# Performance work log

Hardware: AMD Instinct MI355X
Metric: run time of the kernel (lower is better)

Reference implementation:

```python
import jax, jax.numpy as jnp
import numpy as np

K = 9          # number of umbrella neighbors (excluding self)
BN_EPS = 1e-5


def setup_inputs() -> dict:
    key = jax.random.key(0)
    ks = jax.random.split(key, 8)
    B, N, C = 4, 8192, 3
    ch = 7
    x = jax.random.normal(ks[0], (B, N, C), jnp.float32)
    w1 = jax.random.normal(ks[1], (ch, ch), jnp.float32) * 0.4
    gamma1 = jnp.ones((ch,), jnp.float32)
    beta1 = jnp.zeros((ch,), jnp.float32)
    w2 = jax.random.normal(ks[2], (ch, ch), jnp.float32) * 0.4
    bias2 = jax.random.normal(ks[3], (ch,), jnp.float32) * 0.1
    gamma2 = jnp.ones((ch,), jnp.float32)
    beta2 = jnp.zeros((ch,), jnp.float32)
    w3 = jax.random.normal(ks[4], (ch, ch), jnp.float32) * 0.4
    bias3 = jax.random.normal(ks[5], (ch,), jnp.float32) * 0.1
    return dict(x=x, w1=w1, gamma1=gamma1, beta1=beta1, w2=w2, bias2=bias2,
                gamma2=gamma2, beta2=beta2, w3=w3, bias3=bias3)


def _bn(t, gamma, beta):
    # BatchNorm2d in training mode: batch stats over (B, N, K) per channel (last dim)
    m = t.mean(axis=(0, 1, 2))
    v = t.var(axis=(0, 1, 2))  # biased, matching torch BN normalization
    return (t - m) * jax.lax.rsqrt(v + BN_EPS) * gamma + beta


def reference(x, w1, gamma1, beta1, w2, bias2, gamma2, beta2, w3, bias3):
    B, N, _ = x.shape
    # ---- kNN (negative squared distance, top-k largest == nearest) ----
    xsq = jnp.sum(x * x, axis=-1)                       # [B,N]
    xx = jnp.einsum('bnc,bmc->bnm', x, x)               # [B,N,N]
    dist = 2.0 * xx - xsq[:, :, None] - xsq[:, None, :]
    idx = jax.lax.top_k(dist, K + 1)[1]                 # [B,N,K+1], includes self
    # ---- gather neighbor coords, recenter, drop self ----
    nbr = jax.vmap(lambda xb, ib: xb[ib])(x, idx)       # [B,N,K+1,3]
    nbr = nbr - x[:, :, None, :]
    nbr = nbr[:, :, 1:, :]                              # [B,N,K,3]
    # ---- sort neighbors by azimuth phi ----
    phi = jnp.arctan2(nbr[..., 1], nbr[..., 0]) / (2.0 * np.pi) + 0.5
    order = jnp.argsort(phi, axis=-1)                   # [B,N,K]
    srt = jnp.take_along_axis(nbr, order[..., None], axis=2)  # [B,N,K,3]
    # ---- umbrella pairs: (v_i, v_{i+1 mod K}) ----
    v1 = srt
    v2 = jnp.roll(srt, -1, axis=2)
    centroids = 0.5 * (v1 + v2)                         # [B,N,K,3]
    normals = jnp.cross(v1, v2) + 1e-5
    normals = normals / jnp.linalg.norm(normals, axis=-1, keepdims=True)
    # flip so the first normal's x-component is positive (per point)
    pos_mask = (normals[:, :, 0:1, 0] > 0).astype(x.dtype) * 2.0 - 1.0  # [B,N,1]
    normals = normals * pos_mask[..., None]
    positions = jnp.sum(centroids * normals, axis=-1) / jnp.sqrt(jnp.asarray(3.0, x.dtype))
    feat = jnp.concatenate([centroids, normals, positions[..., None]], axis=-1)  # [B,N,K,7]
    # ---- tiny 1x1 conv MLP (channel-last einsum) + BN + ReLU ----
    h = jnp.einsum('bnkc,oc->bnko', feat, w1)
    h = jax.nn.relu(_bn(h, gamma1, beta1))
    h = jnp.einsum('bnkc,oc->bnko', h, w2) + bias2
    h = jax.nn.relu(_bn(h, gamma2, beta2))
    h = jnp.einsum('bnkc,oc->bnko', h, w3) + bias3
    pooled = jnp.max(h, axis=2)                         # [B,N,7]
    return jnp.concatenate([x, pooled], axis=-1)        # [B,N,10]
```

## Files before the change

kernel.cpp:

```cpp
#include <hip/hip_runtime.h>
#include <math.h>

#define BB 4
#define NN 8192
#define TOTAL (BB*NN)
#define KNBR 9
#define CH 7
#define NCHUNK 16
#define CHUNK (NN/NCHUNK)
#define SLOTS 8
#define NROWS (NCHUNK*SLOTS/2)
#define QB 4
#define BN_EPS 1e-5f
#define M_ELEMS (TOTAL*KNBR)
#define NREP 16
#define NBLK 256

#define OFF_PTS   0
#define OFF_PI    524288
#define OFF_STATS 8912896

__device__ __forceinline__ void ibody(float (&dl)[10], int (&il)[10], float d, int ii) {
    bool c0 = d > dl[0];
#pragma unroll
    for (int p = 9; p > 0; p--) {
        bool here = d > dl[p];
        bool up   = d > dl[p-1];
        float nd = up ? dl[p-1] : d;
        int   ni = up ? il[p-1] : ii;
        if (here) { dl[p] = nd; il[p] = ni; }
    }
    if (c0) { dl[0] = d; il[0] = ii; }
}

__device__ __forceinline__ void insert10(float (&dl)[10], int (&il)[10], float d, int ii) {
    if (d > dl[9]) ibody(dl, il, d, ii);
}

__global__ __launch_bounds__(256) void knn_k(const float* __restrict__ x,
                                             float4* __restrict__ pts,
                                             unsigned int* __restrict__ pi,
                                             float* __restrict__ stats) {
    const int b = blockIdx.z, chunk = blockIdx.y;
    const int c0 = chunk * CHUNK;

    if (blockIdx.x == 0 && blockIdx.y == 0 && blockIdx.z == 0) {
        for (int i = threadIdx.x; i < NREP*28 + 8; i += 256) stats[i] = 0.f;
    }

    __shared__ float4 tile[CHUNK];
    if (threadIdx.x < CHUNK/4) {
        const float4* __restrict__ x4 = (const float4*)(x + (long)(b*NN + c0)*3);
        int t = threadIdx.x;
        float4 f0 = x4[3*t], f1 = x4[3*t+1], f2 = x4[3*t+2];
        float px[4] = {f0.x, f0.w, f1.z, f2.y};
        float py[4] = {f0.y, f1.x, f1.w, f2.z};
        float pz[4] = {f0.z, f1.y, f2.x, f2.w};
#pragma unroll
        for (int u = 0; u < 4; u++) {
            float sq = __fadd_rn(__fadd_rn(__fmul_rn(px[u],px[u]), __fmul_rn(py[u],py[u])),
                                 __fmul_rn(pz[u],pz[u]));
            tile[4*t+u] = make_float4(px[u], py[u], pz[u], sq);
        }
    }
    __syncthreads();

    if (blockIdx.x == 0) {
#pragma unroll
        for (int j = 0; j < CHUNK/256; j++)
            pts[b*NN + c0 + threadIdx.x + j*256] = tile[threadIdx.x + j*256];
    }

    const int q0 = blockIdx.x * (256*QB) + threadIdx.x;
    float qx2[QB], qy2[QB], qz2[QB], nqb[QB];
#pragma unroll
    for (int v = 0; v < QB; v++) {
        long qoff = (long)(b*NN + q0 + v*256) * 3;
        float qx = x[qoff], qy = x[qoff+1], qz = x[qoff+2];
        float qw = qx*qx + qy*qy + qz*qz;
        qx2[v] = qx + qx; qy2[v] = qy + qy; qz2[v] = qz + qz;
        nqb[v] = -1.0f - qw;
    }

    unsigned int m[QB][SLOTS];
#pragma unroll
    for (int v = 0; v < QB; v++)
#pragma unroll
        for (int s = 0; s < SLOTS; s++) m[v][s] = 0xFFFFFFFFu;

#pragma unroll 4
    for (int j = 0; j < CHUNK; j++) {
        float4 t = tile[j];
#pragma unroll
        for (int v = 0; v < QB; v++) {
            float d = fmaf(qx2[v], t.x, fmaf(qy2[v], t.y, fmaf(qz2[v], t.z, nqb[v] - t.w)));
            unsigned int kd = (__float_as_uint(d) & 0xFFFFFE00u) | (unsigned int)j;
#pragma unroll
            for (int p = SLOTS-1; p >= 1; p--)
                asm("v_med3_u32 %0, %1, %2, %3" : "=v"(m[v][p]) : "v"(kd), "v"(m[v][p-1]), "v"(m[v][p]));
            m[v][0] = kd < m[v][0] ? kd : m[v][0];
        }
    }

#pragma unroll
    for (int v = 0; v < QB; v++) {
        int idx[SLOTS];
#pragma unroll
        for (int s = 0; s < SLOTS; s++) idx[s] = (int)(m[v][s] & 511u);
#pragma unroll
        for (int r = 0; r < SLOTS; r++) {
#pragma unroll
            for (int i = (r & 1); i + 1 < SLOTS; i += 2) {
                int a = idx[i], c = idx[i+1];
                idx[i] = min(a, c); idx[i+1] = max(a, c);
            }
        }
        int g = b*NN + q0 + v*256;
#pragma unroll
        for (int s2 = 0; s2 < SLOTS/2; s2++) {
            unsigned int lo = (unsigned int)(c0 + idx[2*s2]);
            unsigned int hi = (unsigned int)(c0 + idx[2*s2+1]);
            pi[(long)(chunk*(SLOTS/2) + s2)*TOTAL + g] = lo | (hi << 16);
        }
    }
}

__device__ __forceinline__ void grid_barrier(int* cnt) {
    __syncthreads();
    if (threadIdx.x == 0) {
        __threadfence();
        __hip_atomic_fetch_add(cnt, 1, __ATOMIC_RELEASE, __HIP_MEMORY_SCOPE_AGENT);
        while (__hip_atomic_load(cnt, __ATOMIC_ACQUIRE, __HIP_MEMORY_SCOPE_AGENT) < NBLK)
            __builtin_amdgcn_s_sleep(8);
    }
    __syncthreads();
}

__global__ __launch_bounds__(128, 1) void fused_k(const float* __restrict__ x,
                                                  const float4* __restrict__ pts,
                                                  const unsigned int* __restrict__ pi,
                                                  const float* __restrict__ w1,
                                                  const float* __restrict__ gamma1, const float* __restrict__ beta1,
                                                  const float* __restrict__ w2, const float* __restrict__ bias2,
                                                  const float* __restrict__ gamma2, const float* __restrict__ beta2,
                                                  const float* __restrict__ w3, const float* __restrict__ bias3,
                                                  float* __restrict__ stats, float* __restrict__ out) {
    __shared__ float sw1[49], sw2[49], sw3[49], sb2[7], sb3[7];
    __shared__ float acc[14];
    __shared__ float sco[14];
    if (threadIdx.x < 49) {
        sw1[threadIdx.x] = w1[threadIdx.x];
        sw2[threadIdx.x] = w2[threadIdx.x];
        sw3[threadIdx.x] = w3[threadIdx.x];
    }
    if (threadIdx.x < 7) { sb2[threadIdx.x] = bias2[threadIdx.x]; sb3[threadIdx.x] = bias3[threadIdx.x]; }
    if (threadIdx.x < 14) acc[threadIdx.x] = 0.f;
    __syncthreads();

    int* cnt = (int*)(stats + NREP*28);
    int g = blockIdx.x * 128 + threadIdx.x;
    int b = g >> 13, n = g & (NN-1);
    const float4* __restrict__ base = pts + b*NN;
    float4 qp = base[n];
    float qn = -qp.w;

    float dl[10]; int il[10];
#pragma unroll
    for (int j = 0; j < 10; j++) { dl[j] = -INFINITY; il[j] = 0; }
#pragma unroll
    for (int h = 0; h < 2; h++) {
        unsigned int pk[32];
#pragma unroll
        for (int u = 0; u < 32; u++) pk[u] = pi[(long)(h*32 + u)*TOTAL + g];
#pragma unroll
        for (int bt = 0; bt < 4; bt++) {
            int id[16];
#pragma unroll
            for (int u = 0; u < 8; u++) {
                id[2*u]   = (int)(pk[bt*8 + u] & 0xFFFFu);
                id[2*u+1] = (int)(pk[bt*8 + u] >> 16);
            }
            float4 pp[16];
#pragma unroll
            for (int v = 0; v < 16; v++) pp[v] = base[id[v]];
            float dd[16];
#pragma unroll
            for (int v = 0; v < 16; v++) {
                float dot2 = __fadd_rn(__fadd_rn(__fmul_rn(qp.x, 2.f*pp[v].x),
                                                 __fmul_rn(qp.y, 2.f*pp[v].y)),
                                       __fmul_rn(qp.z, 2.f*pp[v].z));
                dd[v] = __fsub_rn(__fadd_rn(dot2, qn), pp[v].w);
            }
#pragma unroll
            for (int v = 0; v < 16; v++) insert10(dl, il, dd[v], id[v]);
        }
    }

    float vx[9], vy[9], vz[9], ph[9];
#pragma unroll
    for (int t = 0; t < 9; t++) {
        float4 p4 = base[il[t+1]];
        vx[t] = p4.x - qp.x; vy[t] = p4.y - qp.y; vz[t] = p4.z - qp.z;
        ph[t] = atan2f(vy[t], vx[t]) / 6.283185307179586f + 0.5f;
    }

    int rank[9];
#pragma unroll
    for (int t = 0; t < 9; t++) {
        int r = 0;
#pragma unroll
        for (int u = 0; u < 9; u++) {
            if (u == t) continue;
            bool before = (ph[u] < ph[t]) || (ph[u] == ph[t] && u < t);
            r += before ? 1 : 0;
        }
        rank[t] = r;
    }
    float sx[9], sy[9], sz[9];
#pragma unroll
    for (int s = 0; s < 9; s++) {
        float a = 0.f, bb = 0.f, c = 0.f;
#pragma unroll
        for (int t = 0; t < 9; t++) {
            bool m = (rank[t] == s);
            a = m ? vx[t] : a; bb = m ? vy[t] : bb; c = m ? vz[t] : c;
        }
        sx[s] = a; sy[s] = bb; sz[s] = c;
    }

    float sgn;
    {
        float ax = sx[0], ay = sy[0], az = sz[0];
        float bx = sx[1], by = sy[1], bz = sz[1];
        float nx0 = ay*bz - az*by + 1e-5f;
        float ny0 = az*bx - ax*bz + 1e-5f;
        float nz0 = ax*by - ay*bx + 1e-5f;
        float inv = 1.0f / sqrtf(nx0*nx0 + ny0*ny0 + nz0*nz0);
        sgn = (nx0*inv > 0.0f) ? 1.0f : -1.0f;
    }

    float hv[63];
    float sum[7], sumsq[7];
#pragma unroll
    for (int o = 0; o < 7; o++) { sum[o] = 0.f; sumsq[o] = 0.f; }

#pragma unroll
    for (int t = 0; t < 9; t++) {
        const int t2 = (t + 1) % 9;
        float ax = sx[t],  ay = sy[t],  az = sz[t];
        float bx = sx[t2], by = sy[t2], bz = sz[t2];
        float cx = 0.5f*(ax+bx), cy = 0.5f*(ay+by), cz = 0.5f*(az+bz);
        float nx0 = ay*bz - az*by + 1e-5f;
        float ny0 = az*bx - ax*bz + 1e-5f;
        float nz0 = ax*by - ay*bx + 1e-5f;
        float inv = 1.0f / sqrtf(nx0*nx0 + ny0*ny0 + nz0*nz0);
        float nx = nx0*inv*sgn, ny = ny0*inv*sgn, nz = nz0*inv*sgn;
        float pos = (cx*nx + cy*ny + cz*nz) / 1.7320508075688772f;

        float f[7] = {cx, cy, cz, nx, ny, nz, pos};
#pragma unroll
        for (int o = 0; o < 7; o++) {
            float h = 0.f;
#pragma unroll
            for (int c = 0; c < 7; c++) h += f[c] * sw1[o*7 + c];
            hv[t*7 + o] = h;
            sum[o] += h; sumsq[o] += h*h;
        }
    }

#pragma unroll
    for (int o = 0; o < 7; o++) {
        float s  = sum[o];
        float s2 = sumsq[o];
        for (int off = 32; off > 0; off >>= 1) { s += __shfl_down(s, off); s2 += __shfl_down(s2, off); }
        if ((threadIdx.x & 63) == 0) {
            atomicAdd(&acc[o], s);
            atomicAdd(&acc[7 + o], s2);
        }
    }
    __syncthreads();
    if (threadIdx.x < 14)
        atomicAdd(&stats[(blockIdx.x & (NREP-1))*28 + threadIdx.x], acc[threadIdx.x]);

    grid_barrier(&cnt[0]);

    const float invM = 1.0f / (float)M_ELEMS;
    if (threadIdx.x < 7) {
        int c = threadIdx.x;
        float sm = 0.f, sq = 0.f;
#pragma unroll
        for (int r = 0; r < NREP; r++) {
            sm += __hip_atomic_load(&stats[r*28 + c],     __ATOMIC_RELAXED, __HIP_MEMORY_SCOPE_AGENT);
            sq += __hip_atomic_load(&stats[r*28 + 7 + c], __ATOMIC_RELAXED, __HIP_MEMORY_SCOPE_AGENT);
        }
        float m = sm * invM;
        float v = sq * invM - m*m;
        float sc = gamma1[c] / sqrtf(v + BN_EPS);
        sco[c] = sc; sco[7 + c] = beta1[c] - m*sc;
    }
    if (threadIdx.x >= 64 && threadIdx.x < 78) acc[threadIdx.x - 64] = 0.f;
    __syncthreads();

#pragma unroll
    for (int o = 0; o < 7; o++) { sum[o] = 0.f; sumsq[o] = 0.f; }
#pragma unroll
    for (int t = 0; t < 9; t++) {
        float a[7];
#pragma unroll
        for (int c = 0; c < 7; c++) a[c] = fmaxf(hv[t*7 + c]*sco[c] + sco[7 + c], 0.0f);
#pragma unroll
        for (int o = 0; o < 7; o++) {
            float h = 0.f;
#pragma unroll
            for (int c = 0; c < 7; c++) h += a[c] * sw2[o*7 + c];
            h += sb2[o];
            hv[t*7 + o] = h;
            sum[o] += h; sumsq[o] += h*h;
        }
    }
#pragma unroll
    for (int o = 0; o < 7; o++) {
        float s  = sum[o];
        float s2 = sumsq[o];
        for (int off = 32; off > 0; off >>= 1) { s += __shfl_down(s, off); s2 += __shfl_down(s2, off); }
        if ((threadIdx.x & 63) == 0) {
            atomicAdd(&acc[o], s);
            atomicAdd(&acc[7 + o], s2);
        }
    }
    __syncthreads();
    if (threadIdx.x < 14)
        atomicAdd(&stats[(blockIdx.x & (NREP-1))*28 + 14 + threadIdx.x], acc[threadIdx.x]);

    grid_barrier(&cnt[1]);

    if (threadIdx.x < 7) {
        int c = threadIdx.x;
        float sm = 0.f, sq = 0.f;
#pragma unroll
        for (int r = 0; r < NREP; r++) {
            sm += __hip_atomic_load(&stats[r*28 + 14 + c], __ATOMIC_RELAXED, __HIP_MEMORY_SCOPE_AGENT);
            sq += __hip_atomic_load(&stats[r*28 + 21 + c], __ATOMIC_RELAXED, __HIP_MEMORY_SCOPE_AGENT);
        }
        float m = sm * invM;
        float v = sq * invM - m*m;
        float sc = gamma2[c] / sqrtf(v + BN_EPS);
        sco[c] = sc; sco[7 + c] = beta2[c] - m*sc;
    }
    __syncthreads();

    float pooled[7];
#pragma unroll
    for (int o = 0; o < 7; o++) pooled[o] = -INFINITY;
#pragma unroll
    for (int t = 0; t < 9; t++) {
        float a[7];
#pragma unroll
        for (int c = 0; c < 7; c++) a[c] = fmaxf(hv[t*7 + c]*sco[c] + sco[7 + c], 0.0f);
#pragma unroll
        for (int o = 0; o < 7; o++) {
            float h = 0.f;
#pragma unroll
            for (int c = 0; c < 7; c++) h += a[c] * sw3[o*7 + c];
            h += sb3[o];
            pooled[o] = fmaxf(pooled[o], h);
        }
    }
    out[g*10 + 0] = qp.x;
    out[g*10 + 1] = qp.y;
    out[g*10 + 2] = qp.z;
#pragma unroll
    for (int o = 0; o < 7; o++) out[g*10 + 3 + o] = pooled[o];
}

extern "C" void kernel_launch(void* const* d_in, const int* in_sizes, int n_in,
                              void* d_out, int out_size, void* d_ws, size_t ws_size,
                              hipStream_t stream) {
    const float* x      = (const float*)d_in[0];
    const float* w1     = (const float*)d_in[1];
    const float* gamma1 = (const float*)d_in[2];
    const float* beta1  = (const float*)d_in[3];
    const float* w2     = (const float*)d_in[4];
    const float* bias2  = (const float*)d_in[5];
    const float* gamma2 = (const float*)d_in[6];
    const float* beta2  = (const float*)d_in[7];
    const float* w3     = (const float*)d_in[8];
    const float* bias3  = (const float*)d_in[9];
    float* out = (float*)d_out;

    char* ws = (char*)d_ws;
    float4*       pts  = (float4*)(ws + OFF_PTS);
    unsigned int* pi   = (unsigned int*)(ws + OFF_PI);
    float*        stats= (float*)(ws + OFF_STATS);

    knn_k  <<<dim3(NN/(256*QB), NCHUNK, BB), 256, 0, stream>>>(x, pts, pi, stats);
    fused_k<<<NBLK, 128, 0, stream>>>(x, pts, pi, w1, gamma1, beta1, w2, bias2,
                                      gamma2, beta2, w3, bias3, stats, out);
}
```

Baseline: 244.6 us.

## Split fused kernel at first BN barrier, spilling layer-1 activations to workspace

Splits the persistent fused kernel into a geometry kernel that writes first-layer activations to a global buffer and a tail kernel that does the remaining two layers. The first software grid barrier is replaced by a kernel boundary, and the geometry kernel loses its launch-bound occupancy cap of one block. In exchange it writes and re-reads about 9 MB of activations, and it adds a launch. The tail kernel recomputes the BN1 coefficients per thread from stats instead of sharing them through shared memory.

New measurement: 231.8 us. -5.2%, faster.

```diff
diff --git a/kernel.cpp b/kernel.cpp
--- a/kernel.cpp
+++ b/kernel.cpp
@@ -19,6 +19,7 @@
 #define OFF_PTS   0
 #define OFF_PI    524288
 #define OFF_STATS 8912896
+#define OFF_H1    8914944
 
 __device__ __forceinline__ void ibody(float (&dl)[10], int (&il)[10], float d, int ii) {
     bool c0 = d > dl[0];
@@ -125,39 +126,16 @@
     }
 }
 
-__device__ __forceinline__ void grid_barrier(int* cnt) {
-    __syncthreads();
-    if (threadIdx.x == 0) {
-        __threadfence();
-        __hip_atomic_fetch_add(cnt, 1, __ATOMIC_RELEASE, __HIP_MEMORY_SCOPE_AGENT);
-        while (__hip_atomic_load(cnt, __ATOMIC_ACQUIRE, __HIP_MEMORY_SCOPE_AGENT) < NBLK)
-            __builtin_amdgcn_s_sleep(8);
-    }
-    __syncthreads();
-}
-
-__global__ __launch_bounds__(128, 1) void fused_k(const float* __restrict__ x,
-                                                  const float4* __restrict__ pts,
-                                                  const unsigned int* __restrict__ pi,
-                                                  const float* __restrict__ w1,
-                                                  const float* __restrict__ gamma1, const float* __restrict__ beta1,
-                                                  const float* __restrict__ w2, const float* __restrict__ bias2,
-                                                  const float* __restrict__ gamma2, const float* __restrict__ beta2,
-                                                  const float* __restrict__ w3, const float* __restrict__ bias3,
-                                                  float* __restrict__ stats, float* __restrict__ out) {
-    __shared__ float sw1[49], sw2[49], sw3[49], sb2[7], sb3[7];
+__global__ __launch_bounds__(128) void geom_k(const float4* __restrict__ pts,
+                                              const unsigned int* __restrict__ pi,
+                                              const float* __restrict__ w1,
+                                              float* __restrict__ h1, float* __restrict__ stats) {
+    __shared__ float sw1[49];
     __shared__ float acc[14];
-    __shared__ float sco[14];
-    if (threadIdx.x < 49) {
-        sw1[threadIdx.x] = w1[threadIdx.x];
-        sw2[threadIdx.x] = w2[threadIdx.x];
-        sw3[threadIdx.x] = w3[threadIdx.x];
-    }
-    if (threadIdx.x < 7) { sb2[threadIdx.x] = bias2[threadIdx.x]; sb3[threadIdx.x] = bias3[threadIdx.x]; }
+    if (threadIdx.x < 49) sw1[threadIdx.x] = w1[threadIdx.x];
     if (threadIdx.x < 14) acc[threadIdx.x] = 0.f;
     __syncthreads();
 
-    int* cnt = (int*)(stats + NREP*28);
     int g = blockIdx.x * 128 + threadIdx.x;
     int b = g >> 13, n = g & (NN-1);
     const float4* __restrict__ base = pts + b*NN;
@@ -239,7 +217,6 @@
         sgn = (nx0*inv > 0.0f) ? 1.0f : -1.0f;
     }
 
-    float hv[63];
     float sum[7], sumsq[7];
 #pragma unroll
     for (int o = 0; o < 7; o++) { sum[o] = 0.f; sumsq[o] = 0.f; }
@@ -258,12 +235,13 @@
         float pos = (cx*nx + cy*ny + cz*nz) / 1.7320508075688772f;
 
         float f[7] = {cx, cy, cz, nx, ny, nz, pos};
+        float* outp = h1 + ((long)g*9 + t) * 7;
 #pragma unroll
         for (int o = 0; o < 7; o++) {
             float h = 0.f;
 #pragma unroll
             for (int c = 0; c < 7; c++) h += f[c] * sw1[o*7 + c];
-            hv[t*7 + o] = h;
+            outp[o] = h;
             sum[o] += h; sumsq[o] += h*h;
         }
     }
@@ -281,33 +259,60 @@
     __syncthreads();
     if (threadIdx.x < 14)
         atomicAdd(&stats[(blockIdx.x & (NREP-1))*28 + threadIdx.x], acc[threadIdx.x]);
-
-    grid_barrier(&cnt[0]);
-
+}
+
+__device__ __forceinline__ void grid_barrier(int* cnt) {
+    __syncthreads();
+    if (threadIdx.x == 0) {
+        __threadfence();
+        __hip_atomic_fetch_add(cnt, 1, __ATOMIC_RELEASE, __HIP_MEMORY_SCOPE_AGENT);
+        while (__hip_atomic_load(cnt, __ATOMIC_ACQUIRE, __HIP_MEMORY_SCOPE_AGENT) < NBLK)
+            __builtin_amdgcn_s_sleep(8);
+    }
+    __syncthreads();
+}
+
+__global__ __launch_bounds__(128) void tail_k(const float* __restrict__ x,
+                                              const float* __restrict__ h1,
+                                              const float* __restrict__ gamma1, const float* __restrict__ beta1,
+                                              const float* __restrict__ w2, const float* __restrict__ bias2,
+                                              const float* __restrict__ gamma2, const float* __restrict__ beta2,
+                                              const float* __restrict__ w3, const float* __restrict__ bias3,
+                                              float* __restrict__ stats, float* __restrict__ out) {
+    __shared__ float sw2[49], sw3[49], sb2[7], sb3[7];
+    __shared__ float acc[14];
+    __shared__ float sco[14];
+    if (threadIdx.x < 49) { sw2[threadIdx.x] = w2[threadIdx.x]; sw3[threadIdx.x] = w3[threadIdx.x]; }
+    if (threadIdx.x < 7)  { sb2[threadIdx.x] = bias2[threadIdx.x]; sb3[threadIdx.x] = bias3[threadIdx.x]; }
+    if (threadIdx.x < 14) acc[threadIdx.x] = 0.f;
+    __syncthreads();
+
+    int* cnt = (int*)(stats + NREP*28);
+    int g = blockIdx.x * 128 + threadIdx.x;
     const float invM = 1.0f / (float)M_ELEMS;
-    if (threadIdx.x < 7) {
-        int c = threadIdx.x;
+
+    float s1v[7], b1v[7];
+#pragma unroll
+    for (int c = 0; c < 7; c++) {
         float sm = 0.f, sq = 0.f;
 #pragma unroll
-        for (int r = 0; r < NREP; r++) {
-            sm += __hip_atomic_load(&stats[r*28 + c],     __ATOMIC_RELAXED, __HIP_MEMORY_SCOPE_AGENT);
-            sq += __hip_atomic_load(&stats[r*28 + 7 + c], __ATOMIC_RELAXED, __HIP_MEMORY_SCOPE_AGENT);
-        }
+        for (int r = 0; r < NREP; r++) { sm += stats[r*28 + c]; sq += stats[r*28 + 7 + c]; }
         float m = sm * invM;
         float v = sq * invM - m*m;
         float sc = gamma1[c] / sqrtf(v + BN_EPS);
-        sco[c] = sc; sco[7 + c] = beta1[c] - m*sc;
-    }
-    if (threadIdx.x >= 64 && threadIdx.x < 78) acc[threadIdx.x - 64] = 0.f;
-    __syncthreads();
-
+        s1v[c] = sc; b1v[c] = beta1[c] - m*sc;
+    }
+
+    float hv[63];
+    float sum[7], sumsq[7];
 #pragma unroll
     for (int o = 0; o < 7; o++) { sum[o] = 0.f; sumsq[o] = 0.f; }
+    const float* hh = h1 + (long)g * 63;
 #pragma unroll
     for (int t = 0; t < 9; t++) {
         float a[7];
 #pragma unroll
-        for (int c = 0; c < 7; c++) a[c] = fmaxf(hv[t*7 + c]*sco[c] + sco[7 + c], 0.0f);
+        for (int c = 0; c < 7; c++) a[c] = fmaxf(hh[t*7 + c]*s1v[c] + b1v[c], 0.0f);
 #pragma unroll
         for (int o = 0; o < 7; o++) {
             float h = 0.f;
@@ -332,7 +337,7 @@
     if (threadIdx.x < 14)
         atomicAdd(&stats[(blockIdx.x & (NREP-1))*28 + 14 + threadIdx.x], acc[threadIdx.x]);
 
-    grid_barrier(&cnt[1]);
+    grid_barrier(cnt);
 
     if (threadIdx.x < 7) {
         int c = threadIdx.x;
@@ -366,9 +371,9 @@
             pooled[o] = fmaxf(pooled[o], h);
         }
     }
-    out[g*10 + 0] = qp.x;
-    out[g*10 + 1] = qp.y;
-    out[g*10 + 2] = qp.z;
+    out[g*10 + 0] = x[g*3 + 0];
+    out[g*10 + 1] = x[g*3 + 1];
+    out[g*10 + 2] = x[g*3 + 2];
 #pragma unroll
     for (int o = 0; o < 7; o++) out[g*10 + 3 + o] = pooled[o];
 }
@@ -392,8 +397,10 @@
     float4*       pts  = (float4*)(ws + OFF_PTS);
     unsigned int* pi   = (unsigned int*)(ws + OFF_PI);
     float*        stats= (float*)(ws + OFF_STATS);
-
-    knn_k  <<<dim3(NN/(256*QB), NCHUNK, BB), 256, 0, stream>>>(x, pts, pi, stats);
-    fused_k<<<NBLK, 128, 0, stream>>>(x, pts, pi, w1, gamma1, beta1, w2, bias2,
-                                      gamma2, beta2, w3, bias3, stats, out);
-}
+    float*        h1   = (float*)(ws + OFF_H1);
+
+    knn_k <<<dim3(NN/(256*QB), NCHUNK, BB), 256, 0, stream>>>(x, pts, pi, stats);
+    geom_k<<<TOTAL/128, 128, 0, stream>>>(pts, pi, w1, h1, stats);
+    tail_k<<<NBLK, 128, 0, stream>>>(x, h1, gamma1, beta1, w2, bias2,
+                                     gamma2, beta2, w3, bias3, stats, out);
+}
```

## Merge chunk candidates by packed approximate-distance keys before exact rescoring

Applied to the files above, without the earlier changes.

The kNN kernel now writes each chunk's 8 candidates as full 32-bit keys that hold the truncated distance bits plus a 13-bit global index, instead of sorted packed 16-bit index pairs. The second kernel runs a v_med3 selection network over all 128 keys to keep the best 20, then gathers and exactly rescores only those 20 points instead of all 128. This removes most of the random float4 gathers and exact distance computations. In exchange it doubles the candidate buffer written and read, and it relies on the truncated-key preselection never dropping a true top-10 neighbour.

Result: faster. 233.0 us (-4.7%).

```diff
diff --git a/kernel.cpp b/kernel.cpp
--- a/kernel.cpp
+++ b/kernel.cpp
@@ -9,7 +9,8 @@
 #define NCHUNK 16
 #define CHUNK (NN/NCHUNK)
 #define SLOTS 8
-#define NROWS (NCHUNK*SLOTS/2)
+#define NROWS (NCHUNK*SLOTS)
+#define GSEL 20
 #define QB 4
 #define BN_EPS 1e-5f
 #define M_ELEMS (TOTAL*KNBR)
@@ -18,7 +19,7 @@
 
 #define OFF_PTS   0
 #define OFF_PI    524288
-#define OFF_STATS 8912896
+#define OFF_STATS 17301504
 
 __device__ __forceinline__ void ibody(float (&dl)[10], int (&il)[10], float d, int ii) {
     bool c0 = d > dl[0];
@@ -104,23 +105,12 @@
 
 #pragma unroll
     for (int v = 0; v < QB; v++) {
-        int idx[SLOTS];
-#pragma unroll
-        for (int s = 0; s < SLOTS; s++) idx[s] = (int)(m[v][s] & 511u);
-#pragma unroll
-        for (int r = 0; r < SLOTS; r++) {
-#pragma unroll
-            for (int i = (r & 1); i + 1 < SLOTS; i += 2) {
-                int a = idx[i], c = idx[i+1];
-                idx[i] = min(a, c); idx[i+1] = max(a, c);
-            }
-        }
         int g = b*NN + q0 + v*256;
 #pragma unroll
-        for (int s2 = 0; s2 < SLOTS/2; s2++) {
-            unsigned int lo = (unsigned int)(c0 + idx[2*s2]);
-            unsigned int hi = (unsigned int)(c0 + idx[2*s2+1]);
-            pi[(long)(chunk*(SLOTS/2) + s2)*TOTAL + g] = lo | (hi << 16);
+        for (int s = 0; s < SLOTS; s++) {
+            unsigned int mm = m[v][s];
+            unsigned int key = (mm & 0xFFFFE000u) | (unsigned int)(c0 + (int)(mm & 511u));
+            pi[(long)(chunk*SLOTS + s)*TOTAL + g] = key;
         }
     }
 }
@@ -136,15 +126,15 @@
     __syncthreads();
 }
 
-__global__ __launch_bounds__(128, 1) void fused_k(const float* __restrict__ x,
-                                                  const float4* __restrict__ pts,
-                                                  const unsigned int* __restrict__ pi,
-                                                  const float* __restrict__ w1,
-                                                  const float* __restrict__ gamma1, const float* __restrict__ beta1,
-                                                  const float* __restrict__ w2, const float* __restrict__ bias2,
-                                                  const float* __restrict__ gamma2, const float* __restrict__ beta2,
-                                                  const float* __restrict__ w3, const float* __restrict__ bias3,
-                                                  float* __restrict__ stats, float* __restrict__ out) {
+__global__ __launch_bounds__(128) void rest_k(const float* __restrict__ x,
+                                              const float4* __restrict__ pts,
+                                              const unsigned int* __restrict__ pi,
+                                              const float* __restrict__ w1,
+                                              const float* __restrict__ gamma1, const float* __restrict__ beta1,
+                                              const float* __restrict__ w2, const float* __restrict__ bias2,
+                                              const float* __restrict__ gamma2, const float* __restrict__ beta2,
+                                              const float* __restrict__ w3, const float* __restrict__ bias3,
+                                              float* __restrict__ stats, float* __restrict__ out) {
     __shared__ float sw1[49], sw2[49], sw3[49], sb2[7], sb3[7];
     __shared__ float acc[14];
     __shared__ float sco[14];
@@ -153,7 +143,7 @@
         sw2[threadIdx.x] = w2[threadIdx.x];
         sw3[threadIdx.x] = w3[threadIdx.x];
     }
-    if (threadIdx.x < 7) { sb2[threadIdx.x] = bias2[threadIdx.x]; sb3[threadIdx.x] = bias3[threadIdx.x]; }
+    if (threadIdx.x < 7)  { sb2[threadIdx.x] = bias2[threadIdx.x]; sb3[threadIdx.x] = bias3[threadIdx.x]; }
     if (threadIdx.x < 14) acc[threadIdx.x] = 0.f;
     __syncthreads();
 
@@ -164,36 +154,54 @@
     float4 qp = base[n];
     float qn = -qp.w;
 
+    unsigned int mk[GSEL];
+#pragma unroll
+    for (int s = 0; s < GSEL; s++) mk[s] = 0xFFFFFFFFu;
+#pragma unroll
+    for (int h = 0; h < 4; h++) {
+        unsigned int pk[32];
+#pragma unroll
+        for (int u = 0; u < 32; u++) pk[u] = pi[(long)(h*32 + u)*TOTAL + g];
+#pragma unroll
+        for (int u = 0; u < 32; u++) {
+            unsigned int kd = pk[u];
+#pragma unroll
+            for (int p = GSEL-1; p >= 1; p--)
+                asm("v_med3_u32 %0, %1, %2, %3" : "=v"(mk[p]) : "v"(kd), "v"(mk[p-1]), "v"(mk[p]));
+            mk[0] = kd < mk[0] ? kd : mk[0];
+        }
+    }
+
+    int idx[GSEL];
+#pragma unroll
+    for (int s = 0; s < GSEL; s++) idx[s] = (int)(mk[s] & 8191u);
+#pragma unroll
+    for (int r = 0; r < GSEL; r++) {
+#pragma unroll
+        for (int i = (r & 1); i + 1 < GSEL; i += 2) {
+            int a = idx[i], c = idx[i+1];
+            idx[i] = min(a, c); idx[i+1] = max(a, c);
+        }
+    }
+
     float dl[10]; int il[10];
 #pragma unroll
     for (int j = 0; j < 10; j++) { dl[j] = -INFINITY; il[j] = 0; }
 #pragma unroll
-    for (int h = 0; h < 2; h++) {
-        unsigned int pk[32];
-#pragma unroll
-        for (int u = 0; u < 32; u++) pk[u] = pi[(long)(h*32 + u)*TOTAL + g];
-#pragma unroll
-        for (int bt = 0; bt < 4; bt++) {
-            int id[16];
-#pragma unroll
-            for (int u = 0; u < 8; u++) {
-                id[2*u]   = (int)(pk[bt*8 + u] & 0xFFFFu);
-                id[2*u+1] = (int)(pk[bt*8 + u] >> 16);
-            }
-            float4 pp[16];
-#pragma unroll
-            for (int v = 0; v < 16; v++) pp[v] = base[id[v]];
-            float dd[16];
-#pragma unroll
-            for (int v = 0; v < 16; v++) {
-                float dot2 = __fadd_rn(__fadd_rn(__fmul_rn(qp.x, 2.f*pp[v].x),
-                                                 __fmul_rn(qp.y, 2.f*pp[v].y)),
-                                       __fmul_rn(qp.z, 2.f*pp[v].z));
-                dd[v] = __fsub_rn(__fadd_rn(dot2, qn), pp[v].w);
-            }
-#pragma unroll
-            for (int v = 0; v < 16; v++) insert10(dl, il, dd[v], id[v]);
-        }
+    for (int hb = 0; hb < 2; hb++) {
+        float4 pp[10];
+#pragma unroll
+        for (int v = 0; v < 10; v++) pp[v] = base[idx[hb*10 + v]];
+        float dd[10];
+#pragma unroll
+        for (int v = 0; v < 10; v++) {
+            float dot2 = __fadd_rn(__fadd_rn(__fmul_rn(qp.x, 2.f*pp[v].x),
+                                             __fmul_rn(qp.y, 2.f*pp[v].y)),
+                                   __fmul_rn(qp.z, 2.f*pp[v].z));
+            dd[v] = __fsub_rn(__fadd_rn(dot2, qn), pp[v].w);
+        }
+#pragma unroll
+        for (int v = 0; v < 10; v++) insert10(dl, il, dd[v], idx[hb*10 + v]);
     }
 
     float vx[9], vy[9], vz[9], ph[9];
@@ -393,7 +401,7 @@
     unsigned int* pi   = (unsigned int*)(ws + OFF_PI);
     float*        stats= (float*)(ws + OFF_STATS);
 
-    knn_k  <<<dim3(NN/(256*QB), NCHUNK, BB), 256, 0, stream>>>(x, pts, pi, stats);
-    fused_k<<<NBLK, 128, 0, stream>>>(x, pts, pi, w1, gamma1, beta1, w2, bias2,
-                                      gamma2, beta2, w3, bias3, stats, out);
-}
+    knn_k <<<dim3(NN/(256*QB), NCHUNK, BB), 256, 0, stream>>>(x, pts, pi, stats);
+    rest_k<<<NBLK, 128, 0, stream>>>(x, pts, pi, w1, gamma1, beta1, w2, bias2,
+                                     gamma2, beta2, w3, bias3, stats, out);
+}
```
